# Performance work log

Hardware: AMD Instinct MI355X
Metric: run time of the kernel (lower is better)

Reference implementation:

```python
import jax, jax.numpy as jnp
import numpy as np

SIGMA = 2.0  # gaussian kernel std, matches init kwarg
N, H, W = 200, 448, 448
NUM_CLASSES = 80


def setup_inputs() -> dict:
    key = jax.random.key(0)
    k1, k2, k3 = jax.random.split(key, 3)
    seg_masks = (jax.random.uniform(k1, (N, H, W)) < 0.3).astype(jnp.float32)
    # scores in descending order (matrix_nms assumes sorted input)
    cate_scores = jnp.sort(jax.random.uniform(k2, (N,), dtype=jnp.float32))[::-1]
    cate_labels = jax.random.randint(k3, (N,), 0, NUM_CLASSES)
    return {"seg_masks": seg_masks, "cate_scores": cate_scores, "cate_labels": cate_labels}


def reference(seg_masks, cate_scores, cate_labels):
    n = seg_masks.shape[0]
    flat = seg_masks.reshape(n, -1).astype(jnp.float32)          # (n, HW)
    sum_masks = flat.sum(axis=1)                                  # (n,)
    inter = flat @ flat.T                                         # (n, n) mask intersection
    union = sum_masks[None, :] + sum_masks[:, None] - inter
    iou = jnp.triu(inter / union, k=1)                            # upper-tri IoU
    same_label = jnp.triu(
        (cate_labels[None, :] == cate_labels[:, None]).astype(jnp.float32), k=1
    )
    decay_iou = iou * same_label                                  # (n, n)
    # compensate IoU: per-candidate max overlap with a higher-scoring same-class mask
    compensate_iou = decay_iou.max(axis=0)                        # (n,)
    # gaussian decay: exp(-sigma*iou^2) / exp(-sigma*comp_i^2), min over rows
    decay_matrix = jnp.exp(SIGMA * (compensate_iou[:, None] ** 2 - decay_iou ** 2))
    decay_coefficient = decay_matrix.min(axis=0)                  # (n,)
    return cate_scores * decay_coefficient
```

## Files before the change

### kernel.cpp

```cpp
#include <hip/hip_runtime.h>
#include <cstdint>
#include <cstddef>

#define N_INST 200
#define HWPIX (448 * 448)
#define W64 (HWPIX / 64)
#define W16 (HWPIX / 16)
#define SIGMA 2.0f

#define OFF_SUMS  (5017600)
#define OFF_DT    (5018624)

__global__ void zero_kernel(uint32_t* __restrict__ base) {
    int idx = blockIdx.x * blockDim.x + threadIdx.x;
    const int nwords = (1024 + N_INST * N_INST * 4) / 4;
    if (idx < nwords) base[idx] = 0u;
}

__global__ void pack_kernel(const float* __restrict__ seg,
                            uint16_t* __restrict__ packed16,
                            int* __restrict__ sums) {
    const int mask = blockIdx.y;
    const int tid  = threadIdx.x;
    const size_t base = (size_t)mask * HWPIX + (size_t)blockIdx.x * 4096 + (size_t)tid * 16;
    const float4* s4 = (const float4*)(seg + base);
    uint32_t m = 0;
    float4 v0 = s4[0], v1 = s4[1], v2 = s4[2], v3 = s4[3];
    m |= (v0.x > 0.5f) ? 1u << 0  : 0u;  m |= (v0.y > 0.5f) ? 1u << 1  : 0u;
    m |= (v0.z > 0.5f) ? 1u << 2  : 0u;  m |= (v0.w > 0.5f) ? 1u << 3  : 0u;
    m |= (v1.x > 0.5f) ? 1u << 4  : 0u;  m |= (v1.y > 0.5f) ? 1u << 5  : 0u;
    m |= (v1.z > 0.5f) ? 1u << 6  : 0u;  m |= (v1.w > 0.5f) ? 1u << 7  : 0u;
    m |= (v2.x > 0.5f) ? 1u << 8  : 0u;  m |= (v2.y > 0.5f) ? 1u << 9  : 0u;
    m |= (v2.z > 0.5f) ? 1u << 10 : 0u;  m |= (v2.w > 0.5f) ? 1u << 11 : 0u;
    m |= (v3.x > 0.5f) ? 1u << 12 : 0u;  m |= (v3.y > 0.5f) ? 1u << 13 : 0u;
    m |= (v3.z > 0.5f) ? 1u << 14 : 0u;  m |= (v3.w > 0.5f) ? 1u << 15 : 0u;
    packed16[(size_t)mask * W16 + blockIdx.x * 256 + tid] = (uint16_t)m;

    int cnt = __popc(m);
    for (int off = 32; off; off >>= 1) cnt += __shfl_down(cnt, off, 64);
    __shared__ int partial[4];
    int wid = tid >> 6;
    if ((tid & 63) == 0) partial[wid] = cnt;
    __syncthreads();
    if (tid == 0)
        atomicAdd(&sums[mask], partial[0] + partial[1] + partial[2] + partial[3]);
}

#define NTILES 2550

__global__ void pair_kernel(const uint64_t* __restrict__ packed,
                            const int* __restrict__ sums,
                            const int* __restrict__ labels,
                            float* __restrict__ DT) {
    int wt = blockIdx.x * 4 + (threadIdx.x >> 6);
    if (wt >= NTILES) return;
    int lane = threadIdx.x & 63;

    int jt = (int)((sqrtf((float)(4 * wt + 1)) - 1.0f) * 0.5f);
    while ((jt + 1) * (jt + 2) <= wt) ++jt;
    while (jt * (jt + 1) > wt) --jt;
    int it = wt - jt * (jt + 1);
    int i0 = 2 * it;
    int j0 = 4 * jt;

    const uint64_t* A0 = packed + (size_t)i0 * W64;
    const uint64_t* A1 = A0 + W64;
    const uint64_t* B0 = packed + (size_t)j0 * W64;
    const uint64_t* B1 = B0 + W64;
    const uint64_t* B2 = B1 + W64;
    const uint64_t* B3 = B2 + W64;

    int c00 = 0, c01 = 0, c02 = 0, c03 = 0;
    int c10 = 0, c11 = 0, c12 = 0, c13 = 0;
#pragma unroll 7
    for (int iter = 0; iter < 49; ++iter) {
        int k = iter * 64 + lane;
        uint64_t a0 = A0[k], a1 = A1[k];
        uint64_t b0 = B0[k], b1 = B1[k], b2 = B2[k], b3 = B3[k];
        c00 += __popcll(a0 & b0); c01 += __popcll(a0 & b1);
        c02 += __popcll(a0 & b2); c03 += __popcll(a0 & b3);
        c10 += __popcll(a1 & b0); c11 += __popcll(a1 & b1);
        c12 += __popcll(a1 & b2); c13 += __popcll(a1 & b3);
    }
#pragma unroll
    for (int off = 1; off < 64; off <<= 1) {
        c00 += __shfl_xor(c00, off, 64); c01 += __shfl_xor(c01, off, 64);
        c02 += __shfl_xor(c02, off, 64); c03 += __shfl_xor(c03, off, 64);
        c10 += __shfl_xor(c10, off, 64); c11 += __shfl_xor(c11, off, 64);
        c12 += __shfl_xor(c12, off, 64); c13 += __shfl_xor(c13, off, 64);
    }
    if (lane == 0) {
        int cnts[2][4] = {{c00, c01, c02, c03}, {c10, c11, c12, c13}};
#pragma unroll
        for (int r = 0; r < 2; ++r) {
            int i = i0 + r;
            float si = (float)sums[i];
            int li = labels[i];
#pragma unroll
            for (int c = 0; c < 4; ++c) {
                int j = j0 + c;
                if (i < j) {
                    float inter = (float)cnts[r][c];
                    float uni = si + (float)sums[j] - inter;
                    float iou = inter / uni;
                    DT[(size_t)j * N_INST + i] = (li == labels[j]) ? iou : 0.0f;
                }
            }
        }
    }
}

__global__ void comp_kernel(const float* __restrict__ DT,
                            float* __restrict__ comp) {
    int j = blockIdx.x;
    int t = threadIdx.x;
    const float* row = DT + (size_t)j * N_INST;
    float m = 0.0f;
    for (int i = t; i < N_INST; i += 64) m = fmaxf(m, row[i]);
#pragma unroll
    for (int off = 1; off < 64; off <<= 1) m = fmaxf(m, __shfl_xor(m, off, 64));
    if (t == 0) comp[j] = m;
}

__global__ void finalize_kernel(const float* __restrict__ DT,
                                const float* __restrict__ comp,
                                const float* __restrict__ scores,
                                float* __restrict__ out) {
    int j = blockIdx.x;
    int t = threadIdx.x;
    const float* row = DT + (size_t)j * N_INST;
    float m = 3.4e38f;
    for (int i = t; i < N_INST; i += 64) {
        float ci = comp[i];
        float d  = row[i];
        m = fminf(m, ci * ci - d * d);
    }
#pragma unroll
    for (int off = 1; off < 64; off <<= 1) m = fminf(m, __shfl_xor(m, off, 64));
    if (t == 0) out[j] = scores[j] * expf(SIGMA * m);
}

extern "C" void kernel_launch(void* const* d_in, const int* in_sizes, int n_in,
                              void* d_out, int out_size, void* d_ws, size_t ws_size,
                              hipStream_t stream) {
    const float* seg    = (const float*)d_in[0];
    const float* scores = (const float*)d_in[1];
    const int*   labels = (const int*)d_in[2];
    float* out = (float*)d_out;

    uint64_t* packed   = (uint64_t*)d_ws;
    uint16_t* packed16 = (uint16_t*)d_ws;
    int*      sums     = (int*)((char*)d_ws + OFF_SUMS);
    float*    DT       = (float*)((char*)d_ws + OFF_DT);
    float*    comp     = (float*)((char*)d_ws + OFF_SUMS + 800);
    comp = (float*)((char*)d_ws + OFF_DT + (size_t)N_INST * N_INST * 4);

    {
        const int nwords = (1024 + N_INST * N_INST * 4) / 4;
        zero_kernel<<<(nwords + 255) / 256, 256, 0, stream>>>(
            (uint32_t*)((char*)d_ws + OFF_SUMS));
    }
    {
        dim3 grid(49, N_INST);
        pack_kernel<<<grid, 256, 0, stream>>>(seg, packed16, sums);
    }
    pair_kernel<<<(NTILES + 3) / 4, 256, 0, stream>>>(packed, sums, labels, DT);
    comp_kernel<<<N_INST, 64, 0, stream>>>(DT, comp);
    finalize_kernel<<<N_INST, 64, 0, stream>>>(DT, comp, scores, out);
}
```

Before: 263.0 us.

## Use 4x4 pair tiles with K-split chunks and diagonal mask sums

Intersections are now computed on square 4x4 tiles over the upper triangle, with the pixel dimension split into four chunks handled by separate waves. Partial counts go to per-chunk slabs, so no zeroing or atomics are needed. Mask sums are taken from the diagonal tiles, which removes the popcount and atomic from the pack kernel. Pairs of counts are packed into 16-bit halves to halve the shuffle reduction. The comp and finalize kernels are merged into one single-block kernel and an iou kernel is added, trading more launches in the middle for fewer elsewhere and a serial per-thread loop over up to 200 entries.

```diff
diff --git a/kernel.cpp b/kernel.cpp
--- a/kernel.cpp
+++ b/kernel.cpp
@@ -4,28 +4,25 @@
 
 #define N_INST 200
 #define HWPIX (448 * 448)
-#define W64 (HWPIX / 64)
-#define W16 (HWPIX / 16)
+#define W64 3136
+#define W16 12544
 #define SIGMA 2.0f
+#define NCHUNK 4
+#define NTILE 1275
 
-#define OFF_SUMS  (5017600)
-#define OFF_DT    (5018624)
-
-__global__ void zero_kernel(uint32_t* __restrict__ base) {
-    int idx = blockIdx.x * blockDim.x + threadIdx.x;
-    const int nwords = (1024 + N_INST * N_INST * 4) / 4;
-    if (idx < nwords) base[idx] = 0u;
-}
+#define OFF_P   5017600
+#define P_SLAB  (N_INST * N_INST)
+#define OFF_SP  (OFF_P + NCHUNK * P_SLAB * 4)
+#define OFF_DT  (OFF_SP + NCHUNK * 256 * 4)
 
 __global__ void pack_kernel(const float* __restrict__ seg,
-                            uint16_t* __restrict__ packed16,
-                            int* __restrict__ sums) {
+                            uint16_t* __restrict__ packed16) {
     const int mask = blockIdx.y;
     const int tid  = threadIdx.x;
     const size_t base = (size_t)mask * HWPIX + (size_t)blockIdx.x * 4096 + (size_t)tid * 16;
     const float4* s4 = (const float4*)(seg + base);
+    float4 v0 = s4[0], v1 = s4[1], v2 = s4[2], v3 = s4[3];
     uint32_t m = 0;
-    float4 v0 = s4[0], v1 = s4[1], v2 = s4[2], v3 = s4[3];
     m |= (v0.x > 0.5f) ? 1u << 0  : 0u;  m |= (v0.y > 0.5f) ? 1u << 1  : 0u;
     m |= (v0.z > 0.5f) ? 1u << 2  : 0u;  m |= (v0.w > 0.5f) ? 1u << 3  : 0u;
     m |= (v1.x > 0.5f) ? 1u << 4  : 0u;  m |= (v1.y > 0.5f) ? 1u << 5  : 0u;
@@ -35,109 +32,110 @@
     m |= (v3.x > 0.5f) ? 1u << 12 : 0u;  m |= (v3.y > 0.5f) ? 1u << 13 : 0u;
     m |= (v3.z > 0.5f) ? 1u << 14 : 0u;  m |= (v3.w > 0.5f) ? 1u << 15 : 0u;
     packed16[(size_t)mask * W16 + blockIdx.x * 256 + tid] = (uint16_t)m;
-
-    int cnt = __popc(m);
-    for (int off = 32; off; off >>= 1) cnt += __shfl_down(cnt, off, 64);
-    __shared__ int partial[4];
-    int wid = tid >> 6;
-    if ((tid & 63) == 0) partial[wid] = cnt;
-    __syncthreads();
-    if (tid == 0)
-        atomicAdd(&sums[mask], partial[0] + partial[1] + partial[2] + partial[3]);
 }
 
-#define NTILES 2550
+__global__ void pair_kernel(const uint64_t* __restrict__ packed,
+                            int* __restrict__ P,
+                            int* __restrict__ SP) {
+    const int wt   = blockIdx.x * 4 + (threadIdx.x >> 6);
+    const int lane = threadIdx.x & 63;
+    const int t     = wt >> 2;
+    const int chunk = wt & 3;
 
-__global__ void pair_kernel(const uint64_t* __restrict__ packed,
-                            const int* __restrict__ sums,
-                            const int* __restrict__ labels,
-                            float* __restrict__ DT) {
-    int wt = blockIdx.x * 4 + (threadIdx.x >> 6);
-    if (wt >= NTILES) return;
-    int lane = threadIdx.x & 63;
+    int jt = (int)((sqrtf((float)(8 * t + 1)) - 1.0f) * 0.5f);
+    while ((jt + 1) * (jt + 2) / 2 <= t) ++jt;
+    while (jt * (jt + 1) / 2 > t) --jt;
+    const int it = t - jt * (jt + 1) / 2;
+    const int i0 = 4 * it, j0 = 4 * jt;
 
-    int jt = (int)((sqrtf((float)(4 * wt + 1)) - 1.0f) * 0.5f);
-    while ((jt + 1) * (jt + 2) <= wt) ++jt;
-    while (jt * (jt + 1) > wt) --jt;
-    int it = wt - jt * (jt + 1);
-    int i0 = 2 * it;
-    int j0 = 4 * jt;
+    const int ks = (chunk * 49) >> 2;
+    const int ke = ((chunk + 1) * 49) >> 2;
 
-    const uint64_t* A0 = packed + (size_t)i0 * W64;
-    const uint64_t* A1 = A0 + W64;
-    const uint64_t* B0 = packed + (size_t)j0 * W64;
-    const uint64_t* B1 = B0 + W64;
-    const uint64_t* B2 = B1 + W64;
-    const uint64_t* B3 = B2 + W64;
+    const uint64_t* A = packed + (size_t)i0 * W64;
+    const uint64_t* B = packed + (size_t)j0 * W64;
 
-    int c00 = 0, c01 = 0, c02 = 0, c03 = 0;
-    int c10 = 0, c11 = 0, c12 = 0, c13 = 0;
-#pragma unroll 7
-    for (int iter = 0; iter < 49; ++iter) {
-        int k = iter * 64 + lane;
-        uint64_t a0 = A0[k], a1 = A1[k];
-        uint64_t b0 = B0[k], b1 = B1[k], b2 = B2[k], b3 = B3[k];
-        c00 += __popcll(a0 & b0); c01 += __popcll(a0 & b1);
-        c02 += __popcll(a0 & b2); c03 += __popcll(a0 & b3);
-        c10 += __popcll(a1 & b0); c11 += __popcll(a1 & b1);
-        c12 += __popcll(a1 & b2); c13 += __popcll(a1 & b3);
+    int c[16];
+#pragma unroll
+    for (int x = 0; x < 16; ++x) c[x] = 0;
+
+    for (int kb = ks; kb < ke; ++kb) {
+        const int k = kb * 64 + lane;
+        uint64_t a0 = A[k], a1 = A[k + W64], a2 = A[k + 2 * W64], a3 = A[k + 3 * W64];
+        uint64_t b0 = B[k], b1 = B[k + W64], b2 = B[k + 2 * W64], b3 = B[k + 3 * W64];
+        c[0]  += __popcll(a0 & b0); c[1]  += __popcll(a0 & b1);
+        c[2]  += __popcll(a0 & b2); c[3]  += __popcll(a0 & b3);
+        c[4]  += __popcll(a1 & b0); c[5]  += __popcll(a1 & b1);
+        c[6]  += __popcll(a1 & b2); c[7]  += __popcll(a1 & b3);
+        c[8]  += __popcll(a2 & b0); c[9]  += __popcll(a2 & b1);
+        c[10] += __popcll(a2 & b2); c[11] += __popcll(a2 & b3);
+        c[12] += __popcll(a3 & b0); c[13] += __popcll(a3 & b1);
+        c[14] += __popcll(a3 & b2); c[15] += __popcll(a3 & b3);
     }
+
+    int p[8];
+#pragma unroll
+    for (int m = 0; m < 8; ++m) p[m] = c[2 * m] + (c[2 * m + 1] << 16);
 #pragma unroll
     for (int off = 1; off < 64; off <<= 1) {
-        c00 += __shfl_xor(c00, off, 64); c01 += __shfl_xor(c01, off, 64);
-        c02 += __shfl_xor(c02, off, 64); c03 += __shfl_xor(c03, off, 64);
-        c10 += __shfl_xor(c10, off, 64); c11 += __shfl_xor(c11, off, 64);
-        c12 += __shfl_xor(c12, off, 64); c13 += __shfl_xor(c13, off, 64);
+#pragma unroll
+        for (int m = 0; m < 8; ++m) p[m] += __shfl_xor(p[m], off, 64);
     }
+
     if (lane == 0) {
-        int cnts[2][4] = {{c00, c01, c02, c03}, {c10, c11, c12, c13}};
 #pragma unroll
-        for (int r = 0; r < 2; ++r) {
-            int i = i0 + r;
-            float si = (float)sums[i];
-            int li = labels[i];
+        for (int r = 0; r < 4; ++r) {
 #pragma unroll
-            for (int c = 0; c < 4; ++c) {
-                int j = j0 + c;
-                if (i < j) {
-                    float inter = (float)cnts[r][c];
-                    float uni = si + (float)sums[j] - inter;
-                    float iou = inter / uni;
-                    DT[(size_t)j * N_INST + i] = (li == labels[j]) ? iou : 0.0f;
-                }
+            for (int cc = 0; cc < 4; ++cc) {
+                const int idx = r * 4 + cc;
+                const int val = (idx & 1) ? (int)(((unsigned)p[idx >> 1]) >> 16)
+                                          : (p[idx >> 1] & 0xFFFF);
+                const int i = i0 + r, j = j0 + cc;
+                if (i < j)       P[chunk * P_SLAB + j * N_INST + i] = val;
+                else if (i == j) SP[chunk * 256 + i] = val;
             }
         }
     }
 }
 
-__global__ void comp_kernel(const float* __restrict__ DT,
-                            float* __restrict__ comp) {
-    int j = blockIdx.x;
-    int t = threadIdx.x;
-    const float* row = DT + (size_t)j * N_INST;
-    float m = 0.0f;
-    for (int i = t; i < N_INST; i += 64) m = fmaxf(m, row[i]);
-#pragma unroll
-    for (int off = 1; off < 64; off <<= 1) m = fmaxf(m, __shfl_xor(m, off, 64));
-    if (t == 0) comp[j] = m;
+__global__ void iou_kernel(const int* __restrict__ P,
+                           const int* __restrict__ SP,
+                           const int* __restrict__ labels,
+                           float* __restrict__ DTf) {
+    const int j = blockIdx.x;
+    const int sj = SP[j] + SP[256 + j] + SP[512 + j] + SP[768 + j];
+    const int lj = labels[j];
+    for (int i = threadIdx.x; i < j; i += 64) {
+        const int inter = P[j * N_INST + i] + P[P_SLAB + j * N_INST + i]
+                        + P[2 * P_SLAB + j * N_INST + i] + P[3 * P_SLAB + j * N_INST + i];
+        const int si = SP[i] + SP[256 + i] + SP[512 + i] + SP[768 + i];
+        const float iou = (float)inter / (float)(si + sj - inter);
+        DTf[j * N_INST + i] = (labels[i] == lj) ? iou : 0.0f;
+    }
 }
 
-__global__ void finalize_kernel(const float* __restrict__ DT,
-                                const float* __restrict__ comp,
+__global__ void finalize_kernel(const float* __restrict__ DTf,
                                 const float* __restrict__ scores,
                                 float* __restrict__ out) {
-    int j = blockIdx.x;
-    int t = threadIdx.x;
-    const float* row = DT + (size_t)j * N_INST;
-    float m = 3.4e38f;
-    for (int i = t; i < N_INST; i += 64) {
-        float ci = comp[i];
-        float d  = row[i];
-        m = fminf(m, ci * ci - d * d);
+    __shared__ float comp[N_INST];
+    const int t = threadIdx.x;
+    if (t < N_INST) {
+        const float* row = DTf + (size_t)t * N_INST;
+        float m = 0.0f;
+        for (int i = 0; i < t; ++i) m = fmaxf(m, row[i]);
+        comp[t] = m;
     }
-#pragma unroll
-    for (int off = 1; off < 64; off <<= 1) m = fminf(m, __shfl_xor(m, off, 64));
-    if (t == 0) out[j] = scores[j] * expf(SIGMA * m);
+    __syncthreads();
+    if (t < N_INST) {
+        const float* row = DTf + (size_t)t * N_INST;
+        float mn = 3.4e38f;
+        for (int i = 0; i < N_INST; ++i) {
+            const float ci = comp[i];
+            float v = ci * ci;
+            if (i < t) { const float d = row[i]; v -= d * d; }
+            mn = fminf(mn, v);
+        }
+        out[t] = scores[t] * expf(SIGMA * mn);
+    }
 }
 
 extern "C" void kernel_launch(void* const* d_in, const int* in_sizes, int n_in,
@@ -150,21 +148,15 @@
 
     uint64_t* packed   = (uint64_t*)d_ws;
     uint16_t* packed16 = (uint16_t*)d_ws;
-    int*      sums     = (int*)((char*)d_ws + OFF_SUMS);
-    float*    DT       = (float*)((char*)d_ws + OFF_DT);
-    float*    comp     = (float*)((char*)d_ws + OFF_SUMS + 800);
-    comp = (float*)((char*)d_ws + OFF_DT + (size_t)N_INST * N_INST * 4);
+    int*      P        = (int*)((char*)d_ws + OFF_P);
+    int*      SP       = (int*)((char*)d_ws + OFF_SP);
+    float*    DTf      = (float*)((char*)d_ws + OFF_DT);
 
     {
-        const int nwords = (1024 + N_INST * N_INST * 4) / 4;
-        zero_kernel<<<(nwords + 255) / 256, 256, 0, stream>>>(
-            (uint32_t*)((char*)d_ws + OFF_SUMS));
+        dim3 grid(49, N_INST);
+        pack_kernel<<<grid, 256, 0, stream>>>(seg, packed16);
     }
-    {
-        dim3 grid(49, N_INST);
-        pack_kernel<<<grid, 256, 0, stream>>>(seg, packed16, sums);
-    }
-    pair_kernel<<<(NTILES + 3) / 4, 256, 0, stream>>>(packed, sums, labels, DT);
-    comp_kernel<<<N_INST, 64, 0, stream>>>(DT, comp);
-    finalize_kernel<<<N_INST, 64, 0, stream>>>(DT, comp, scores, out);
+    pair_kernel<<<NTILE, 256, 0, stream>>>(packed, P, SP);
+    iou_kernel<<<N_INST, 64, 0, stream>>>(P, SP, labels, DTf);
+    finalize_kernel<<<1, 256, 0, stream>>>(DTf, scores, out);
 }
```

Result: slower. 290.7 us (+10.5%).
